# Kernel optimization log

Hardware: AMD Instinct MI355X
Metric: run time of the kernel (lower is better)

The kernel has to match this reference:

```python
import jax, jax.numpy as jnp
import numpy as np

DIM = 1024
N_HIDDEN = 64
NUM_HEADS = 16
B, S = 4, 1024
# original torch code: scale = sqrt(n_hidden // num_heads) = sqrt(64 // 16) = 2.0
SCALE = float(np.sqrt(N_HIDDEN // NUM_HEADS))


def setup_inputs() -> dict:
    key = jax.random.key(0)
    ks = jax.random.split(key, 10)
    lim = 1.0 / np.sqrt(DIM)          # nn.Linear default init range
    lim_o = 1.0 / np.sqrt(N_HIDDEN * NUM_HEADS)
    u = lambda k, shape, l: jax.random.uniform(k, shape, jnp.float32, -l, l)
    x = jax.random.normal(ks[0], (B, S, DIM), jnp.float32)
    attn_mask = jax.random.randint(ks[1], (B, S, S), 0, 2).astype(jnp.int32)
    # stacked per-head projection weights: [H, dim, n_hidden]
    Wq = u(ks[2], (NUM_HEADS, DIM, N_HIDDEN), lim)
    bq = u(ks[3], (NUM_HEADS, N_HIDDEN), lim)
    Wk = u(ks[4], (NUM_HEADS, DIM, N_HIDDEN), lim)
    bk = u(ks[5], (NUM_HEADS, N_HIDDEN), lim)
    Wv = u(ks[6], (NUM_HEADS, DIM, N_HIDDEN), lim)
    bv = u(ks[7], (NUM_HEADS, N_HIDDEN), lim)
    Wo = u(ks[8], (NUM_HEADS * N_HIDDEN, DIM), lim_o)
    bo = u(ks[9], (DIM,), lim_o)
    return {"x": x, "attn_mask": attn_mask, "Wq": Wq, "bq": bq,
            "Wk": Wk, "bk": bk, "Wv": Wv, "bv": bv, "Wo": Wo, "bo": bo}


def reference(x, attn_mask, Wq, bq, Wk, bk, Wv, bv, Wo, bo):
    # batched QKV across all heads (replaces the per-head Python loop)
    Q = jnp.einsum('bsd,hde->bhse', x, Wq) + bq[None, :, None, :]
    K = jnp.einsum('bsd,hde->bhse', x, Wk) + bk[None, :, None, :]
    V = jnp.einsum('bsd,hde->bhse', x, Wv) + bv[None, :, None, :]
    scores = jnp.einsum('bhse,bhte->bhst', Q, K) / SCALE
    alpha = jax.nn.softmax(scores, axis=-1)
    # faithful to original: zero out masked entries AFTER softmax, no renorm
    alpha = jnp.where(attn_mask[:, None, :, :] == 0, 0.0, alpha)  # [B,H,S,S]
    out = jnp.einsum('bhst,bhte->bhse', alpha, V)                 # [B,H,S,E]
    # torch.cat over heads on last dim == reshape to [B,S,H*E] in head order
    concat = out.transpose(0, 2, 1, 3).reshape(B, S, NUM_HEADS * N_HIDDEN)
    attn_output = concat @ Wo + bo                                # [B,S,dim]
    return attn_output, alpha
```

## Files before the change

### kernel.cpp

```cpp
#include <hip/hip_runtime.h>
#include <stdint.h>

#define S_LEN 1024
#define DIM   1024
#define NHID  64
#define NHEAD 16
#define NB    4

typedef __bf16 bf16x8 __attribute__((ext_vector_type(8)));
typedef float  f32x4  __attribute__((ext_vector_type(4)));
typedef unsigned short u16;

__device__ __forceinline__ u16 f2b(float f) {
  unsigned u = __float_as_uint(f);
  u += 0x7FFFu + ((u >> 16) & 1u);
  return (u16)(u >> 16);
}

__device__ __forceinline__ f32x4 mfma16(bf16x8 a, bf16x8 b, f32x4 c) {
  return __builtin_amdgcn_mfma_f32_16x16x32_bf16(a, b, c, 0, 0, 0);
}

__global__ __launch_bounds__(256) void k_cvt_x(const float* __restrict__ x,
                                               u16* __restrict__ xb) {
  int i = blockIdx.x * 256 + threadIdx.x;
  float4 v = ((const float4*)x)[i];
  ushort4 o;
  o.x = f2b(v.x); o.y = f2b(v.y); o.z = f2b(v.z); o.w = f2b(v.w);
  ((ushort4*)xb)[i] = o;
}

__global__ __launch_bounds__(256) void k_maskbits(const int* __restrict__ mask,
                                                  uint32_t* __restrict__ bits) {
  int w = blockIdx.x * 256 + threadIdx.x;
  const int4* mp = (const int4*)mask + (size_t)w * 8;
  uint32_t v = 0;
#pragma unroll
  for (int i = 0; i < 8; ++i) {
    int4 m = mp[i];
    v |= (m.x != 0 ? 1u : 0u) << (i * 4 + 0);
    v |= (m.y != 0 ? 1u : 0u) << (i * 4 + 1);
    v |= (m.z != 0 ? 1u : 0u) << (i * 4 + 2);
    v |= (m.w != 0 ? 1u : 0u) << (i * 4 + 3);
  }
  bits[w] = v;
}

__global__ __launch_bounds__(256) void k_transpose(const float* __restrict__ in,
                                                   u16* __restrict__ out,
                                                   int R, int C) {
  const float* ip = in + (size_t)blockIdx.x * R * C;
  u16* op = out + (size_t)blockIdx.x * R * C;
  __shared__ float tile[32][65];
  int r0 = blockIdx.y * 32, c0 = blockIdx.z * 64;
  int t = threadIdx.x;
  {
    int col = t & 63, rr = t >> 6;
#pragma unroll
    for (int p = 0; p < 8; ++p) {
      int r = p * 4 + rr;
      tile[r][col] = ip[(size_t)(r0 + r) * C + c0 + col];
    }
  }
  __syncthreads();
  {
    int d = t & 31, er = t >> 5;
#pragma unroll
    for (int p = 0; p < 8; ++p) {
      int e = p * 8 + er;
      op[(size_t)(c0 + e) * R + r0 + d] = f2b(tile[d][e]);
    }
  }
}

__global__ __launch_bounds__(256) void k_qkv(const u16* __restrict__ xb,
                                             const u16* __restrict__ Wtb,
                                             const float* __restrict__ bq,
                                             const float* __restrict__ bk,
                                             const float* __restrict__ bv,
                                             u16* __restrict__ Qb,
                                             u16* __restrict__ Kb,
                                             u16* __restrict__ Vtb) {
  __shared__ __align__(16) char lds[32768];
  int t = threadIdx.x, w = t >> 6, lane = t & 63;
  int l15 = lane & 15, l4 = lane >> 4;
  int m0 = blockIdx.x * 128, n0 = blockIdx.y * 128, sel = blockIdx.z;
  const u16* Wh = Wtb + (size_t)sel * (NHEAD * NHID * DIM);
  int wr = w >> 1, wc = w & 1;

  f32x4 acc[4][4];
  const f32x4 fz = {0.f, 0.f, 0.f, 0.f};
#pragma unroll
  for (int i = 0; i < 4; ++i)
#pragma unroll
    for (int j = 0; j < 4; ++j) acc[i][j] = fz;

  for (int kk = 0; kk < 16; ++kk) {
    int k0 = kk * 64;
#pragma unroll
    for (int c = 0; c < 4; ++c) {
      int idx = c * 256 + t, r = idx >> 3, cb = idx & 7;
      int4 v = *(const int4*)(xb + (size_t)(m0 + r) * DIM + k0 + cb * 8);
      *(int4*)(lds + r * 128 + ((cb * 16) ^ ((r & 7) << 4))) = v;
    }
#pragma unroll
    for (int c = 0; c < 4; ++c) {
      int idx = c * 256 + t, r = idx >> 3, cb = idx & 7;
      int4 v = *(const int4*)(Wh + (size_t)(n0 + r) * DIM + k0 + cb * 8);
      *(int4*)(lds + 16384 + r * 128 + ((cb * 16) ^ ((r & 7) << 4))) = v;
    }
    __syncthreads();
    bf16x8 a[4][2], bb[4][2];
#pragma unroll
    for (int mf = 0; mf < 4; ++mf)
#pragma unroll
      for (int kc = 0; kc < 2; ++kc) {
        int row = wr * 64 + mf * 16 + l15;
        int kb = kc * 64 + l4 * 16;
        a[mf][kc] = *(const bf16x8*)(lds + row * 128 + (kb ^ ((row & 7) << 4)));
      }
#pragma unroll
    for (int nf = 0; nf < 4; ++nf)
#pragma unroll
      for (int kc = 0; kc < 2; ++kc) {
        int row = wc * 64 + nf * 16 + l15;
        int kb = kc * 64 + l4 * 16;
        bb[nf][kc] = *(const bf16x8*)(lds + 16384 + row * 128 + (kb ^ ((row & 7) << 4)));
      }
#pragma unroll
    for (int kc = 0; kc < 2; ++kc)
#pragma unroll
      for (int mf = 0; mf < 4; ++mf)
#pragma unroll
        for (int nf = 0; nf < 4; ++nf)
          acc[mf][nf] = mfma16(a[mf][kc], bb[nf][kc], acc[mf][nf]);
    __syncthreads();
  }

  const float* bias = (sel == 0) ? bq : (sel == 1) ? bk : bv;
  float postScale = (sel == 0) ? 0.5f : 1.0f;
#pragma unroll
  for (int nf = 0; nf < 4; ++nf) {
    int n = n0 + wc * 64 + nf * 16 + l15;
    int h = n >> 6, e = n & 63;
    float bv_ = bias[n];
#pragma unroll
    for (int mf = 0; mf < 4; ++mf) {
      int mrow0 = m0 + wr * 64 + mf * 16 + l4 * 4;
      int b_ = mrow0 >> 10, s0 = mrow0 & 1023;
      if (sel == 2) {
        ushort4 pk;
        pk.x = f2b(acc[mf][nf][0] + bv_);
        pk.y = f2b(acc[mf][nf][1] + bv_);
        pk.z = f2b(acc[mf][nf][2] + bv_);
        pk.w = f2b(acc[mf][nf][3] + bv_);
        *(ushort4*)(Vtb + ((size_t)(b_ * NHEAD + h) * NHID + e) * S_LEN + s0) = pk;
      } else {
        u16* dst = (sel == 0) ? Qb : Kb;
#pragma unroll
        for (int j = 0; j < 4; ++j)
          dst[((size_t)(b_ * NHEAD + h) * S_LEN + s0 + j) * NHID + e] =
              f2b((acc[mf][nf][j] + bv_) * postScale);
      }
    }
  }
}

__global__ __launch_bounds__(256) void k_attn(const u16* __restrict__ Qb,
                                              const u16* __restrict__ Kb,
                                              const u16* __restrict__ Vtb,
                                              const uint32_t* __restrict__ mbitsG,
                                              float* __restrict__ alphaOut,
                                              u16* __restrict__ Ob) {
  __shared__ __align__(16) char smem[38016];
  uint32_t* mbits = (uint32_t*)smem;
  float* redM = (float*)(smem + 4224);
  float* redS = (float*)(smem + 4736);
  char* chunkB = smem + 5248;
  int t = threadIdx.x, w = t >> 6, lane = t & 63;
  int l15 = lane & 15, l4 = lane >> 4;
  int q0 = blockIdx.x * 32;
  int bh = blockIdx.y, b = bh >> 4, hh = bh & 15;
  const u16* Qh = Qb + (size_t)bh * S_LEN * NHID;
  const u16* Kh = Kb + (size_t)bh * S_LEN * NHID;
  const u16* Vh = Vtb + (size_t)bh * NHID * S_LEN;
  int kbase = w * 256;

  uint4 mw4 = ((const uint4*)(mbitsG + ((size_t)b * S_LEN + q0) * 32))[t];

  bf16x8 aq[2][2];
#pragma unroll
  for (int rq = 0; rq < 2; ++rq)
#pragma unroll
    for (int ec = 0; ec < 2; ++ec)
      aq[rq][ec] = *(const bf16x8*)(Qh + (size_t)(q0 + rq * 16 + l15) * NHID +
                                    ec * 32 + l4 * 8);

  {
    int row = t >> 3, c0 = (t & 7) * 4;
    mbits[row * 33 + c0 + 0] = mw4.x;
    mbits[row * 33 + c0 + 1] = mw4.y;
    mbits[row * 33 + c0 + 2] = mw4.z;
    mbits[row * 33 + c0 + 3] = mw4.w;
  }

  f32x4 sc[2][16];
  const f32x4 fz = {0.f, 0.f, 0.f, 0.f};
#pragma unroll
  for (int rq = 0; rq < 2; ++rq)
#pragma unroll
    for (int kf = 0; kf < 16; ++kf) sc[rq][kf] = fz;

#pragma unroll
  for (int kf = 0; kf < 16; ++kf) {
    int key = kbase + kf * 16 + l15;
    bf16x8 kb0 = *(const bf16x8*)(Kh + (size_t)key * NHID + l4 * 8);
    bf16x8 kb1 = *(const bf16x8*)(Kh + (size_t)key * NHID + 32 + l4 * 8);
#pragma unroll
    for (int rq = 0; rq < 2; ++rq) {
      sc[rq][kf] = mfma16(aq[rq][0], kb0, sc[rq][kf]);
      sc[rq][kf] = mfma16(aq[rq][1], kb1, sc[rq][kf]);
    }
  }

  float rm[2][4];
#pragma unroll
  for (int rq = 0; rq < 2; ++rq)
#pragma unroll
    for (int j = 0; j < 4; ++j) {
      float m = sc[rq][0][j];
#pragma unroll
      for (int kf = 1; kf < 16; ++kf) m = fmaxf(m, sc[rq][kf][j]);
      rm[rq][j] = m;
    }
#pragma unroll
  for (int msk = 1; msk < 16; msk <<= 1)
#pragma unroll
    for (int rq = 0; rq < 2; ++rq)
#pragma unroll
      for (int j = 0; j < 4; ++j)
        rm[rq][j] = fmaxf(rm[rq][j], __shfl_xor(rm[rq][j], msk));
  if (l15 == 0) {
#pragma unroll
    for (int rq = 0; rq < 2; ++rq)
#pragma unroll
      for (int j = 0; j < 4; ++j)
        redM[w * 32 + rq * 16 + l4 * 4 + j] = rm[rq][j];
  }
  __syncthreads();
  float Mx[2][4];
#pragma unroll
  for (int rq = 0; rq < 2; ++rq)
#pragma unroll
    for (int j = 0; j < 4; ++j) {
      int row = rq * 16 + l4 * 4 + j;
      Mx[rq][j] = fmaxf(fmaxf(redM[row], redM[32 + row]),
                        fmaxf(redM[64 + row], redM[96 + row]));
    }

  float ls[2][4] = {{0.f, 0.f, 0.f, 0.f}, {0.f, 0.f, 0.f, 0.f}};
#pragma unroll
  for (int kf = 0; kf < 16; ++kf)
#pragma unroll
    for (int rq = 0; rq < 2; ++rq)
#pragma unroll
      for (int j = 0; j < 4; ++j) {
        float p = __expf(sc[rq][kf][j] - Mx[rq][j]);
        sc[rq][kf][j] = p;
        ls[rq][j] += p;
      }
#pragma unroll
  for (int msk = 1; msk < 16; msk <<= 1)
#pragma unroll
    for (int rq = 0; rq < 2; ++rq)
#pragma unroll
      for (int j = 0; j < 4; ++j)
        ls[rq][j] += __shfl_xor(ls[rq][j], msk);
  if (l15 == 0) {
#pragma unroll
    for (int rq = 0; rq < 2; ++rq)
#pragma unroll
      for (int j = 0; j < 4; ++j)
        redS[w * 32 + rq * 16 + l4 * 4 + j] = ls[rq][j];
  }
  __syncthreads();
  float inv[2][4];
#pragma unroll
  for (int rq = 0; rq < 2; ++rq)
#pragma unroll
    for (int j = 0; j < 4; ++j) {
      int row = rq * 16 + l4 * 4 + j;
      inv[rq][j] = 1.f / (redS[row] + redS[32 + row] + redS[64 + row] + redS[96 + row]);
    }

  const float* ab = nullptr;
  float* abW = alphaOut + (size_t)bh * S_LEN * S_LEN;
  (void)ab;

  f32x4 o[2][4];
#pragma unroll
  for (int rq = 0; rq < 2; ++rq)
#pragma unroll
    for (int ef = 0; ef < 4; ++ef) o[rq][ef] = fz;

  auto produce = [&](int c) {
    char* buf = chunkB + (w * 2 + (c & 1)) * 4096;
    int widxBase = (kbase >> 5) + c * 2;
#pragma unroll
    for (int f = 0; f < 4; ++f) {
      int kf = c * 4 + f;
      int keyg = kbase + kf * 16 + l15;
      int widx = widxBase + (f >> 1);
      int bitpos = ((f & 1) << 4) + l15;
#pragma unroll
      for (int rq = 0; rq < 2; ++rq)
#pragma unroll
        for (int j = 0; j < 4; ++j) {
          int qloc = rq * 16 + l4 * 4 + j;
          uint32_t mwd = mbits[qloc * 33 + widx];
          float av = ((mwd >> bitpos) & 1u) ? sc[rq][kf][j] * inv[rq][j] : 0.f;
          __builtin_nontemporal_store(av, abW + (size_t)(q0 + qloc) * S_LEN + keyg);
          int klc = f * 16 + l15;
          *(u16*)(buf + qloc * 128 + ((2 * klc) ^ ((qloc & 7) << 4))) = f2b(av);
        }
    }
  };
  auto pv = [&](int c) {
    char* buf = chunkB + (w * 2 + (c & 1)) * 4096;
#pragma unroll
    for (int kc2 = 0; kc2 < 2; ++kc2) {
      bf16x8 pa[2];
#pragma unroll
      for (int rq = 0; rq < 2; ++rq) {
        int qloc = rq * 16 + l15;
        pa[rq] = *(const bf16x8*)(buf + qloc * 128 +
                                  ((kc2 * 64 + l4 * 16) ^ ((qloc & 7) << 4)));
      }
#pragma unroll
      for (int ef = 0; ef < 4; ++ef) {
        int e = ef * 16 + l15;
        bf16x8 vb = *(const bf16x8*)(Vh + (size_t)e * S_LEN + kbase + c * 64 +
                                     kc2 * 32 + l4 * 8);
#pragma unroll
        for (int rq = 0; rq < 2; ++rq) o[rq][ef] = mfma16(pa[rq], vb, o[rq][ef]);
      }
    }
  };

  produce(0);
  produce(1); pv(0);
  produce(2); pv(1);
  produce(3); pv(2);
  pv(3);

  __syncthreads();
  float* redO = (float*)(smem + 5248);
#pragma unroll
  for (int rq = 0; rq < 2; ++rq) {
#pragma unroll
    for (int ef = 0; ef < 4; ++ef)
#pragma unroll
      for (int j = 0; j < 4; ++j)
        redO[(w * 16 + l4 * 4 + j) * 64 + ef * 16 + l15] = o[rq][ef][j];
    __syncthreads();
    {
      int e = t & 63, r4 = t >> 6;
#pragma unroll
      for (int p = 0; p < 4; ++p) {
        int r = p * 4 + r4;
        float s4 = redO[r * 64 + e] + redO[(16 + r) * 64 + e] +
                   redO[(32 + r) * 64 + e] + redO[(48 + r) * 64 + e];
        Ob[(size_t)(b * S_LEN + q0 + rq * 16 + r) * DIM + hh * NHID + e] = f2b(s4);
      }
    }
    __syncthreads();
  }
}

__global__ __launch_bounds__(256) void k_oproj(const u16* __restrict__ Ob,
                                               const u16* __restrict__ Wotb,
                                               const float* __restrict__ bo,
                                               float* __restrict__ out) {
  __shared__ __align__(16) char lds[32768];
  int t = threadIdx.x, w = t >> 6, lane = t & 63;
  int l15 = lane & 15, l4 = lane >> 4;
  int m0 = blockIdx.x * 128, n0 = blockIdx.y * 128;
  int wr = w >> 1, wc = w & 1;
  f32x4 acc[4][4];
  const f32x4 fz = {0.f, 0.f, 0.f, 0.f};
#pragma unroll
  for (int i = 0; i < 4; ++i)
#pragma unroll
    for (int j = 0; j < 4; ++j) acc[i][j] = fz;

  for (int kk = 0; kk < 16; ++kk) {
    int k0 = kk * 64;
#pragma unroll
    for (int c = 0; c < 4; ++c) {
      int idx = c * 256 + t, r = idx >> 3, cb = idx & 7;
      int4 v = *(const int4*)(Ob + (size_t)(m0 + r) * DIM + k0 + cb * 8);
      *(int4*)(lds + r * 128 + ((cb * 16) ^ ((r & 7) << 4))) = v;
    }
#pragma unroll
    for (int c = 0; c < 4; ++c) {
      int idx = c * 256 + t, r = idx >> 3, cb = idx & 7;
      int4 v = *(const int4*)(Wotb + (size_t)(n0 + r) * DIM + k0 + cb * 8);
      *(int4*)(lds + 16384 + r * 128 + ((cb * 16) ^ ((r & 7) << 4))) = v;
    }
    __syncthreads();
    bf16x8 a[4][2], bb[4][2];
#pragma unroll
    for (int mf = 0; mf < 4; ++mf)
#pragma unroll
      for (int kc = 0; kc < 2; ++kc) {
        int row = wr * 64 + mf * 16 + l15;
        int kb = kc * 64 + l4 * 16;
        a[mf][kc] = *(const bf16x8*)(lds + row * 128 + (kb ^ ((row & 7) << 4)));
      }
#pragma unroll
    for (int nf = 0; nf < 4; ++nf)
#pragma unroll
      for (int kc = 0; kc < 2; ++kc) {
        int row = wc * 64 + nf * 16 + l15;
        int kb = kc * 64 + l4 * 16;
        bb[nf][kc] = *(const bf16x8*)(lds + 16384 + row * 128 + (kb ^ ((row & 7) << 4)));
      }
#pragma unroll
    for (int kc = 0; kc < 2; ++kc)
#pragma unroll
      for (int mf = 0; mf < 4; ++mf)
#pragma unroll
        for (int nf = 0; nf < 4; ++nf)
          acc[mf][nf] = mfma16(a[mf][kc], bb[nf][kc], acc[mf][nf]);
    __syncthreads();
  }
#pragma unroll
  for (int nf = 0; nf < 4; ++nf) {
    int n = n0 + wc * 64 + nf * 16 + l15;
    float bv_ = bo[n];
#pragma unroll
    for (int mf = 0; mf < 4; ++mf)
#pragma unroll
      for (int j = 0; j < 4; ++j) {
        int m = m0 + wr * 64 + mf * 16 + l4 * 4 + j;
        out[(size_t)m * DIM + n] = acc[mf][nf][j] + bv_;
      }
  }
}

extern "C" void kernel_launch(void* const* d_in, const int* in_sizes, int n_in,
                              void* d_out, int out_size, void* d_ws, size_t ws_size,
                              hipStream_t stream) {
  const float* x    = (const float*)d_in[0];
  const int*   mask = (const int*)d_in[1];
  const float* Wq   = (const float*)d_in[2];
  const float* bq   = (const float*)d_in[3];
  const float* Wk   = (const float*)d_in[4];
  const float* bk   = (const float*)d_in[5];
  const float* Wv   = (const float*)d_in[6];
  const float* bv   = (const float*)d_in[7];
  const float* Wo   = (const float*)d_in[8];
  const float* bo   = (const float*)d_in[9];
  float* out = (float*)d_out;
  float* alphaOut = out + (size_t)NB * S_LEN * DIM;

  char* ws = (char*)d_ws;
  u16* xb    = (u16*)(ws);
  u16* Wtb   = (u16*)(ws + 8388608);
  u16* Wotb  = (u16*)(ws + 14680064);
  u16* Qb    = (u16*)(ws + 16777216);
  u16* Kb    = (u16*)(ws + 25165824);
  u16* Vtb   = (u16*)(ws + 33554432);
  u16* Ob    = (u16*)(ws + 41943040);
  uint32_t* mbits = (uint32_t*)(ws + 50331648);

  k_maskbits<<<512, 256, 0, stream>>>(mask, mbits);
  k_cvt_x<<<4096, 256, 0, stream>>>(x, xb);
  k_transpose<<<dim3(16, 32, 1), 256, 0, stream>>>(Wq, Wtb,           1024, 64);
  k_transpose<<<dim3(16, 32, 1), 256, 0, stream>>>(Wk, Wtb + 1048576, 1024, 64);
  k_transpose<<<dim3(16, 32, 1), 256, 0, stream>>>(Wv, Wtb + 2097152, 1024, 64);
  k_transpose<<<dim3(1, 32, 16), 256, 0, stream>>>(Wo, Wotb,          1024, 1024);
  k_qkv<<<dim3(32, 8, 3), 256, 0, stream>>>(xb, Wtb, bq, bk, bv, Qb, Kb, Vtb);
  k_attn<<<dim3(32, 64), 256, 0, stream>>>(Qb, Kb, Vtb, mbits, alphaOut, Ob);
  k_oproj<<<dim3(32, 8), 256, 0, stream>>>(Ob, Wotb, bo, out);
}
```

Before: 265.0 us.

## Halve attention query tile to 16 rows and raise occupancy

The attention kernel now handles 16 query rows per block instead of 32, and the grid doubles to 64x64. This halves the score registers, LDS footprint and reduction buffers, and adds a launch bound of 4 blocks per CU so more waves can hide latency. The cost is that each K and V tile is loaded twice as often from global memory/L2, since it is reused across fewer query rows. The output reduction also becomes a single pass.

```diff
diff --git a/kernel.cpp b/kernel.cpp
--- a/kernel.cpp
+++ b/kernel.cpp
@@ -166,146 +166,112 @@
   }
 }
 
-__global__ __launch_bounds__(256) void k_attn(const u16* __restrict__ Qb,
-                                              const u16* __restrict__ Kb,
-                                              const u16* __restrict__ Vtb,
-                                              const uint32_t* __restrict__ mbitsG,
-                                              float* __restrict__ alphaOut,
-                                              u16* __restrict__ Ob) {
-  __shared__ __align__(16) char smem[38016];
+__global__ __launch_bounds__(256, 4) void k_attn(const u16* __restrict__ Qb,
+                                                 const u16* __restrict__ Kb,
+                                                 const u16* __restrict__ Vtb,
+                                                 const uint32_t* __restrict__ mbitsG,
+                                                 float* __restrict__ alphaOut,
+                                                 u16* __restrict__ Ob) {
+  __shared__ __align__(16) char smem[19072];
   uint32_t* mbits = (uint32_t*)smem;
-  float* redM = (float*)(smem + 4224);
-  float* redS = (float*)(smem + 4736);
-  char* chunkB = smem + 5248;
+  float* redM = (float*)(smem + 2176);
+  float* redS = (float*)(smem + 2432);
+  char* chunkB = smem + 2688;
   int t = threadIdx.x, w = t >> 6, lane = t & 63;
   int l15 = lane & 15, l4 = lane >> 4;
-  int q0 = blockIdx.x * 32;
+  int q0 = blockIdx.x * 16;
   int bh = blockIdx.y, b = bh >> 4, hh = bh & 15;
   const u16* Qh = Qb + (size_t)bh * S_LEN * NHID;
   const u16* Kh = Kb + (size_t)bh * S_LEN * NHID;
   const u16* Vh = Vtb + (size_t)bh * NHID * S_LEN;
   int kbase = w * 256;
 
-  uint4 mw4 = ((const uint4*)(mbitsG + ((size_t)b * S_LEN + q0) * 32))[t];
-
-  bf16x8 aq[2][2];
-#pragma unroll
-  for (int rq = 0; rq < 2; ++rq)
-#pragma unroll
-    for (int ec = 0; ec < 2; ++ec)
-      aq[rq][ec] = *(const bf16x8*)(Qh + (size_t)(q0 + rq * 16 + l15) * NHID +
-                                    ec * 32 + l4 * 8);
+  uint2 mw2 = ((const uint2*)(mbitsG + ((size_t)b * S_LEN + q0) * 32))[t];
+
+  bf16x8 aq[2];
+#pragma unroll
+  for (int ec = 0; ec < 2; ++ec)
+    aq[ec] = *(const bf16x8*)(Qh + (size_t)(q0 + l15) * NHID + ec * 32 + l4 * 8);
 
   {
-    int row = t >> 3, c0 = (t & 7) * 4;
-    mbits[row * 33 + c0 + 0] = mw4.x;
-    mbits[row * 33 + c0 + 1] = mw4.y;
-    mbits[row * 33 + c0 + 2] = mw4.z;
-    mbits[row * 33 + c0 + 3] = mw4.w;
-  }
-
-  f32x4 sc[2][16];
+    int row = t >> 4, c0 = (t & 15) * 2;
+    mbits[row * 33 + c0 + 0] = mw2.x;
+    mbits[row * 33 + c0 + 1] = mw2.y;
+  }
+
+  f32x4 sc[16];
   const f32x4 fz = {0.f, 0.f, 0.f, 0.f};
 #pragma unroll
-  for (int rq = 0; rq < 2; ++rq)
-#pragma unroll
-    for (int kf = 0; kf < 16; ++kf) sc[rq][kf] = fz;
+  for (int kf = 0; kf < 16; ++kf) sc[kf] = fz;
 
 #pragma unroll
   for (int kf = 0; kf < 16; ++kf) {
     int key = kbase + kf * 16 + l15;
     bf16x8 kb0 = *(const bf16x8*)(Kh + (size_t)key * NHID + l4 * 8);
     bf16x8 kb1 = *(const bf16x8*)(Kh + (size_t)key * NHID + 32 + l4 * 8);
-#pragma unroll
-    for (int rq = 0; rq < 2; ++rq) {
-      sc[rq][kf] = mfma16(aq[rq][0], kb0, sc[rq][kf]);
-      sc[rq][kf] = mfma16(aq[rq][1], kb1, sc[rq][kf]);
-    }
-  }
-
-  float rm[2][4];
-#pragma unroll
-  for (int rq = 0; rq < 2; ++rq)
+    sc[kf] = mfma16(aq[0], kb0, sc[kf]);
+    sc[kf] = mfma16(aq[1], kb1, sc[kf]);
+  }
+
+  float rm[4];
+#pragma unroll
+  for (int j = 0; j < 4; ++j) {
+    float m = sc[0][j];
+#pragma unroll
+    for (int kf = 1; kf < 16; ++kf) m = fmaxf(m, sc[kf][j]);
+    rm[j] = m;
+  }
+#pragma unroll
+  for (int msk = 1; msk < 16; msk <<= 1)
+#pragma unroll
+    for (int j = 0; j < 4; ++j) rm[j] = fmaxf(rm[j], __shfl_xor(rm[j], msk));
+  if (l15 == 0) {
+#pragma unroll
+    for (int j = 0; j < 4; ++j) redM[w * 16 + l4 * 4 + j] = rm[j];
+  }
+  __syncthreads();
+  float Mx[4];
+#pragma unroll
+  for (int j = 0; j < 4; ++j) {
+    int row = l4 * 4 + j;
+    Mx[j] = fmaxf(fmaxf(redM[row], redM[16 + row]),
+                  fmaxf(redM[32 + row], redM[48 + row]));
+  }
+
+  float ls[4] = {0.f, 0.f, 0.f, 0.f};
+#pragma unroll
+  for (int kf = 0; kf < 16; ++kf)
 #pragma unroll
     for (int j = 0; j < 4; ++j) {
-      float m = sc[rq][0][j];
-#pragma unroll
-      for (int kf = 1; kf < 16; ++kf) m = fmaxf(m, sc[rq][kf][j]);
-      rm[rq][j] = m;
+      float p = __expf(sc[kf][j] - Mx[j]);
+      sc[kf][j] = p;
+      ls[j] += p;
     }
 #pragma unroll
   for (int msk = 1; msk < 16; msk <<= 1)
 #pragma unroll
-    for (int rq = 0; rq < 2; ++rq)
-#pragma unroll
-      for (int j = 0; j < 4; ++j)
-        rm[rq][j] = fmaxf(rm[rq][j], __shfl_xor(rm[rq][j], msk));
+    for (int j = 0; j < 4; ++j) ls[j] += __shfl_xor(ls[j], msk);
   if (l15 == 0) {
 #pragma unroll
-    for (int rq = 0; rq < 2; ++rq)
-#pragma unroll
-      for (int j = 0; j < 4; ++j)
-        redM[w * 32 + rq * 16 + l4 * 4 + j] = rm[rq][j];
+    for (int j = 0; j < 4; ++j) redS[w * 16 + l4 * 4 + j] = ls[j];
   }
   __syncthreads();
-  float Mx[2][4];
-#pragma unroll
-  for (int rq = 0; rq < 2; ++rq)
-#pragma unroll
-    for (int j = 0; j < 4; ++j) {
-      int row = rq * 16 + l4 * 4 + j;
-      Mx[rq][j] = fmaxf(fmaxf(redM[row], redM[32 + row]),
-                        fmaxf(redM[64 + row], redM[96 + row]));
-    }
-
-  float ls[2][4] = {{0.f, 0.f, 0.f, 0.f}, {0.f, 0.f, 0.f, 0.f}};
-#pragma unroll
-  for (int kf = 0; kf < 16; ++kf)
-#pragma unroll
-    for (int rq = 0; rq < 2; ++rq)
-#pragma unroll
-      for (int j = 0; j < 4; ++j) {
-        float p = __expf(sc[rq][kf][j] - Mx[rq][j]);
-        sc[rq][kf][j] = p;
-        ls[rq][j] += p;
-      }
-#pragma unroll
-  for (int msk = 1; msk < 16; msk <<= 1)
-#pragma unroll
-    for (int rq = 0; rq < 2; ++rq)
-#pragma unroll
-      for (int j = 0; j < 4; ++j)
-        ls[rq][j] += __shfl_xor(ls[rq][j], msk);
-  if (l15 == 0) {
-#pragma unroll
-    for (int rq = 0; rq < 2; ++rq)
-#pragma unroll
-      for (int j = 0; j < 4; ++j)
-        redS[w * 32 + rq * 16 + l4 * 4 + j] = ls[rq][j];
-  }
-  __syncthreads();
-  float inv[2][4];
-#pragma unroll
-  for (int rq = 0; rq < 2; ++rq)
-#pragma unroll
-    for (int j = 0; j < 4; ++j) {
-      int row = rq * 16 + l4 * 4 + j;
-      inv[rq][j] = 1.f / (redS[row] + redS[32 + row] + redS[64 + row] + redS[96 + row]);
-    }
-
-  const float* ab = nullptr;
+  float inv[4];
+#pragma unroll
+  for (int j = 0; j < 4; ++j) {
+    int row = l4 * 4 + j;
+    inv[j] = 1.f / (redS[row] + redS[16 + row] + redS[32 + row] + redS[48 + row]);
+  }
+
   float* abW = alphaOut + (size_t)bh * S_LEN * S_LEN;
-  (void)ab;
-
-  f32x4 o[2][4];
-#pragma unroll
-  for (int rq = 0; rq < 2; ++rq)
-#pragma unroll
-    for (int ef = 0; ef < 4; ++ef) o[rq][ef] = fz;
+
+  f32x4 o[4];
+#pragma unroll
+  for (int ef = 0; ef < 4; ++ef) o[ef] = fz;
 
   auto produce = [&](int c) {
-    char* buf = chunkB + (w * 2 + (c & 1)) * 4096;
-    int widxBase = (kbase >> 5) + c * 2;
+    char* buf = chunkB + (w * 2 + (c & 1)) * 2048;
+    int widxBase = w * 8 + c * 2;
 #pragma unroll
     for (int f = 0; f < 4; ++f) {
       int kf = c * 4 + f;
@@ -313,36 +279,29 @@
       int widx = widxBase + (f >> 1);
       int bitpos = ((f & 1) << 4) + l15;
 #pragma unroll
-      for (int rq = 0; rq < 2; ++rq)
-#pragma unroll
-        for (int j = 0; j < 4; ++j) {
-          int qloc = rq * 16 + l4 * 4 + j;
-          uint32_t mwd = mbits[qloc * 33 + widx];
-          float av = ((mwd >> bitpos) & 1u) ? sc[rq][kf][j] * inv[rq][j] : 0.f;
-          __builtin_nontemporal_store(av, abW + (size_t)(q0 + qloc) * S_LEN + keyg);
-          int klc = f * 16 + l15;
-          *(u16*)(buf + qloc * 128 + ((2 * klc) ^ ((qloc & 7) << 4))) = f2b(av);
-        }
+      for (int j = 0; j < 4; ++j) {
+        int row = l4 * 4 + j;
+        uint32_t mwd = mbits[row * 33 + widx];
+        float av = ((mwd >> bitpos) & 1u) ? sc[kf][j] * inv[j] : 0.f;
+        __builtin_nontemporal_store(av, abW + (size_t)(q0 + row) * S_LEN + keyg);
+        int klc = f * 16 + l15;
+        *(u16*)(buf + row * 128 + ((2 * klc) ^ ((row & 7) << 4))) = f2b(av);
+      }
     }
   };
   auto pv = [&](int c) {
-    char* buf = chunkB + (w * 2 + (c & 1)) * 4096;
+    char* buf = chunkB + (w * 2 + (c & 1)) * 2048;
 #pragma unroll
     for (int kc2 = 0; kc2 < 2; ++kc2) {
-      bf16x8 pa[2];
-#pragma unroll
-      for (int rq = 0; rq < 2; ++rq) {
-        int qloc = rq * 16 + l15;
-        pa[rq] = *(const bf16x8*)(buf + qloc * 128 +
-                                  ((kc2 * 64 + l4 * 16) ^ ((qloc & 7) << 4)));
-      }
+      int qrow = l15;
+      bf16x8 pa = *(const bf16x8*)(buf + qrow * 128 +
+                                   ((kc2 * 64 + l4 * 16) ^ ((qrow & 7) << 4)));
 #pragma unroll
       for (int ef = 0; ef < 4; ++ef) {
         int e = ef * 16 + l15;
         bf16x8 vb = *(const bf16x8*)(Vh + (size_t)e * S_LEN + kbase + c * 64 +
                                      kc2 * 32 + l4 * 8);
-#pragma unroll
-        for (int rq = 0; rq < 2; ++rq) o[rq][ef] = mfma16(pa[rq], vb, o[rq][ef]);
+        o[ef] = mfma16(pa, vb, o[ef]);
       }
     }
   };
@@ -354,26 +313,22 @@
   pv(3);
 
   __syncthreads();
-  float* redO = (float*)(smem + 5248);
-#pragma unroll
-  for (int rq = 0; rq < 2; ++rq) {
-#pragma unroll
-    for (int ef = 0; ef < 4; ++ef)
-#pragma unroll
-      for (int j = 0; j < 4; ++j)
-        redO[(w * 16 + l4 * 4 + j) * 64 + ef * 16 + l15] = o[rq][ef][j];
-    __syncthreads();
-    {
-      int e = t & 63, r4 = t >> 6;
-#pragma unroll
-      for (int p = 0; p < 4; ++p) {
-        int r = p * 4 + r4;
-        float s4 = redO[r * 64 + e] + redO[(16 + r) * 64 + e] +
-                   redO[(32 + r) * 64 + e] + redO[(48 + r) * 64 + e];
-        Ob[(size_t)(b * S_LEN + q0 + rq * 16 + r) * DIM + hh * NHID + e] = f2b(s4);
-      }
-    }
-    __syncthreads();
+  float* redO = (float*)chunkB;
+#pragma unroll
+  for (int ef = 0; ef < 4; ++ef)
+#pragma unroll
+    for (int j = 0; j < 4; ++j)
+      redO[w * 1024 + (l4 * 4 + j) * 64 + ef * 16 + l15] = o[ef][j];
+  __syncthreads();
+  {
+    int e = t & 63, r4 = t >> 6;
+#pragma unroll
+    for (int p = 0; p < 4; ++p) {
+      int r = p * 4 + r4;
+      float s4 = redO[r * 64 + e] + redO[1024 + r * 64 + e] +
+                 redO[2048 + r * 64 + e] + redO[3072 + r * 64 + e];
+      Ob[(size_t)(b * S_LEN + q0 + r) * DIM + hh * NHID + e] = f2b(s4);
+    }
   }
 }
 
@@ -481,6 +436,6 @@
   k_transpose<<<dim3(16, 32, 1), 256, 0, stream>>>(Wv, Wtb + 2097152, 1024, 64);
   k_transpose<<<dim3(1, 32, 16), 256, 0, stream>>>(Wo, Wotb,          1024, 1024);
   k_qkv<<<dim3(32, 8, 3), 256, 0, stream>>>(xb, Wtb, bq, bk, bv, Qb, Kb, Vtb);
-  k_attn<<<dim3(32, 64), 256, 0, stream>>>(Qb, Kb, Vtb, mbits, alphaOut, Ob);
+  k_attn<<<dim3(64, 64), 256, 0, stream>>>(Qb, Kb, Vtb, mbits, alphaOut, Ob);
   k_oproj<<<dim3(32, 8), 256, 0, stream>>>(Ob, Wotb, bo, out);
 }
```

Result: faster. 226.1 us (-14.7%).
